# Optimization experiments

Hardware: AMD Instinct MI355X
Metric: run time of the kernel (lower is better)

The kernel has to match this reference:

```python
import jax, jax.numpy as jnp
from jax import lax
import numpy as np

B, N = 64, 128           # graphs per batch, nodes per graph
MAX_LEVEL = 3
N_TRUNKS, TRUNK_LEN = 32, 32
H, OUT = 256, 10


def setup_inputs() -> dict:
    key = jax.random.key(0)
    ks = jax.random.split(key, 12)
    batch_feature = jax.random.normal(ks[0], (B, N), dtype=jnp.float32)
    trunk_idx = jax.random.randint(ks[1], (MAX_LEVEL, N_TRUNKS, TRUNK_LEN), 0, N, dtype=jnp.int32)
    trunk_len = jax.random.randint(ks[2], (MAX_LEVEL, N_TRUNKS), 1, TRUNK_LEN + 1, dtype=jnp.int32)
    s = 1.0 / np.sqrt(H)
    W_enc = jax.random.uniform(ks[3], (1, H), jnp.float32, -1.0, 1.0)
    b_enc = jax.random.uniform(ks[4], (H,), jnp.float32, -1.0, 1.0)
    W_ih = jax.random.uniform(ks[5], (MAX_LEVEL, 4 * H, H), jnp.float32, -s, s)
    W_hh = jax.random.uniform(ks[6], (MAX_LEVEL, 4 * H, H), jnp.float32, -s, s)
    b_ih = jax.random.uniform(ks[7], (MAX_LEVEL, 4 * H), jnp.float32, -s, s)
    b_hh = jax.random.uniform(ks[8], (MAX_LEVEL, 4 * H), jnp.float32, -s, s)
    W_lin = jax.random.uniform(ks[9], (MAX_LEVEL, H, OUT), jnp.float32, -s, s)
    b_lin = jax.random.uniform(ks[10], (MAX_LEVEL, OUT), jnp.float32, -s, s)
    return {"batch_feature": batch_feature, "trunk_idx": trunk_idx, "trunk_len": trunk_len,
            "W_enc": W_enc, "b_enc": b_enc, "W_ih": W_ih, "W_hh": W_hh,
            "b_ih": b_ih, "b_hh": b_hh, "W_lin": W_lin, "b_lin": b_lin}


def _lstm_scan(seq, W_ih, W_hh, b):
    """seq: [L, M, H] -> all hidden states [L, M, H] (single-layer LSTM, PyTorch gate order i,f,g,o)."""
    M = seq.shape[1]
    Hd = W_hh.shape[1]
    def step(carry, x_t):
        h, c = carry
        gates = x_t @ W_ih.T + h @ W_hh.T + b   # [M, 4H]
        i, f, g, o = jnp.split(gates, 4, axis=-1)
        c = jax.nn.sigmoid(f) * c + jax.nn.sigmoid(i) * jnp.tanh(g)
        h = jax.nn.sigmoid(o) * jnp.tanh(c)
        return (h, c), h
    init = (jnp.zeros((M, Hd), seq.dtype), jnp.zeros((M, Hd), seq.dtype))
    _, hs = lax.scan(step, init, seq)
    return hs


def reference(batch_feature, trunk_idx, trunk_len, W_enc, b_enc, W_ih, W_hh, b_ih, b_hh, W_lin, b_lin):
    Bv, Nv = batch_feature.shape
    Hd = W_enc.shape[1]
    # node encoder on scalar features: x [B*N, 1] @ W_enc [1, H]
    x_attr = (batch_feature.reshape(-1, 1) @ W_enc + b_enc).reshape(Bv, Nv, Hd)
    trunk_len = jnp.maximum(trunk_len, 1)
    score = jnp.zeros((Bv, W_lin.shape[-1]), x_attr.dtype)
    for l in range(trunk_idx.shape[0]):
        idx = trunk_idx[l]                       # [T, L]
        T, L = idx.shape
        seqs = x_attr[:, idx]                    # gather trunks -> [B, T, L, H]
        seqs = seqs.reshape(Bv * T, L, Hd).transpose(1, 0, 2)   # [L, B*T, H]
        hs = _lstm_scan(seqs, W_ih[l], W_hh[l], b_ih[l] + b_hh[l])  # [L, B*T, H]
        lens = jnp.tile(trunk_len[l], Bv)        # [B*T]
        h_last = hs[lens - 1, jnp.arange(Bv * T)]   # hidden at last valid step (== packed h_n)
        h_trunk = h_last.reshape(Bv, T, Hd).sum(axis=1)  # scatter-sum per graph (indices are i repeated T times)
        score = score + h_trunk @ W_lin[l] + b_lin[l]
    return score


if __name__ == "__main__":
    out = reference(**setup_inputs())
    print(out.shape, out.dtype)
```

## Files before the change

kernel.cpp:

```cpp
#include <hip/hip_runtime.h>
#include <hip/hip_bf16.h>
#include <stdint.h>

#define B_   64
#define N_   128
#define H_   256
#define FH   1024
#define NT   32
#define TL   32
#define LV   3
#define OUT_ 10
#define NTRK 96
#define UNITS 384
#define NWORK 256

typedef __attribute__((ext_vector_type(4))) int   int4v;
typedef __attribute__((ext_vector_type(4))) float f32x4;

#define QW  (0.0625f / 127.0f)
#define QH  (1.0f / 127.0f)
#define QS  (QW * QH)
#define L2E 1.442695041f
#define QSI (-L2E * QS)
#define QSG (2.0f * L2E * QS)
#define C2  (2.0f * L2E)

__device__ inline float exp2f_(float x) { return __builtin_amdgcn_exp2f(x); }
__device__ inline float rcpf_(float x)  { return __builtin_amdgcn_rcpf(x); }

__global__ void prep_all(const float* __restrict__ W_enc, const float* __restrict__ b_enc,
                         const float* __restrict__ W_ih, const float* __restrict__ b_ih,
                         const float* __restrict__ b_hh, const float* __restrict__ W_hh,
                         const float* __restrict__ b_lin, const int* __restrict__ trunk_len,
                         float* __restrict__ u, float* __restrict__ v,
                         char* __restrict__ whh_i8, float* __restrict__ out,
                         int* __restrict__ sorted, int* __restrict__ counter) {
    int blk = blockIdx.x;
    int tid = threadIdx.x;
    if (blk < 768) {
        int j = blk * 4 + (tid >> 6);
        int lane = tid & 63;
        const float4 w  = ((const float4*)(W_ih + (size_t)j * H_))[lane];
        const float4 we = ((const float4*)W_enc)[lane];
        const float4 be = ((const float4*)b_enc)[lane];
        float du = w.x * we.x + w.y * we.y + w.z * we.z + w.w * we.w;
        float dv = w.x * be.x + w.y * be.y + w.z * be.z + w.w * be.w;
        for (int m = 32; m >= 1; m >>= 1) { du += __shfl_xor(du, m); dv += __shfl_xor(dv, m); }
        if (lane == 0) {
            int g = (j & 1023) >> 8;
            float s = (g == 2) ? (2.0f * L2E) : (-L2E);
            u[j] = s * du;
            v[j] = s * (dv + b_ih[j] + b_hh[j]);
        }
    } else if (blk < 1536) {
        int gid = (blk - 768) * 256 + tid;
        const float4 w = ((const float4*)W_hh)[gid];
        char4 o;
        int a0 = __float2int_rn(w.x * (127.0f / 0.0625f));
        int a1 = __float2int_rn(w.y * (127.0f / 0.0625f));
        int a2 = __float2int_rn(w.z * (127.0f / 0.0625f));
        int a3 = __float2int_rn(w.w * (127.0f / 0.0625f));
        a0 = a0 > 127 ? 127 : (a0 < -127 ? -127 : a0);
        a1 = a1 > 127 ? 127 : (a1 < -127 ? -127 : a1);
        a2 = a2 > 127 ? 127 : (a2 < -127 ? -127 : a2);
        a3 = a3 > 127 ? 127 : (a3 < -127 ? -127 : a3);
        o.x = (char)a0; o.y = (char)a1; o.z = (char)a2; o.w = (char)a3;
        ((char4*)whh_i8)[gid] = o;
        if (gid < B_ * OUT_) {
            int oo = gid % OUT_;
            out[gid] = b_lin[oo] + b_lin[OUT_ + oo] + b_lin[2 * OUT_ + oo];
        }
    } else {
        if (tid < NTRK) {
            int li = trunk_len[tid]; if (li < 1) li = 1;
            int rank = 0;
            for (int j2 = 0; j2 < NTRK; ++j2) {
                int lj = trunk_len[j2]; if (lj < 1) lj = 1;
                rank += (lj > li) || (lj == li && j2 < tid);
            }
            sorted[rank] = tid;
        }
        if (tid == 0) *counter = 0;
    }
}

__global__ __launch_bounds__(1024) __attribute__((amdgpu_waves_per_eu(4, 4)))
void lstm_main(const float* __restrict__ bfeat, const int* __restrict__ trunk_idx,
               const int* __restrict__ trunk_len,
               const char* __restrict__ whh_i8,
               const float* __restrict__ u, const float* __restrict__ v,
               const float* __restrict__ W_lin, const int* __restrict__ sorted,
               int* __restrict__ counter, float* __restrict__ out) {
    __shared__ __align__(16) char hbuf[2][16][272];
    __shared__ __align__(16) float sbuf[2][16];
    __shared__ int sh_uid;

    const int tid = threadIdx.x;
    const int w = tid >> 6;
    const int lane = tid & 63;
    const int col = lane & 15;
    const int q = lane >> 4;

    int4v z4; z4[0] = 0; z4[1] = 0; z4[2] = 0; z4[3] = 0;
    asm volatile("" : "+v"(z4));

    for (;;) {
        if (tid == 0) sh_uid = atomicAdd(counter, 1);
        __syncthreads();
        const int uid = sh_uid;
        if (uid >= UNITS) break;

        const int r = uid >> 2, qq = uid & 3;
        const int tt = sorted[r];
        const int l = tt >> 5;
        const int b0 = qq * 16;

        int len = trunk_len[tt];
        if (len < 1) len = 1;
        const int* tix = trunk_idx + tt * TL;
        const char* whh_l = whh_i8 + (size_t)l * FH * H_;

        int4v Breg[4][4];
        #pragma unroll
        for (int g = 0; g < 4; ++g) {
            int j = g * 256 + w * 16 + col;
            const char* bp = whh_l + (size_t)j * H_ + q * 16;
            #pragma unroll
            for (int k = 0; k < 4; ++k)
                Breg[g][k] = *(const int4v*)(bp + k * 64);
        }

        float u_r[4], v_r[4];
        {
            const float* u_l = u + l * FH;
            const float* v_l = v + l * FH;
            #pragma unroll
            for (int g = 0; g < 4; ++g) {
                int j = g * 256 + w * 16 + col;
                u_r[g] = u_l[j];
                v_r[g] = v_l[j];
            }
        }

        float c_r[4];

        if (tid < 16) sbuf[0][tid] = bfeat[(b0 + tid) * N_ + tix[0]];
        __syncthreads();

        {
            if (len > 1 && tid < 16) sbuf[1][tid] = bfeat[(b0 + tid) * N_ + tix[1]];
            f32x4 sv = *(const f32x4*)&sbuf[0][q * 4];
            #pragma unroll
            for (int rg = 0; rg < 4; ++rg) {
                float xi = fmaf(sv[rg], u_r[0], v_r[0]);
                float xg = fmaf(sv[rg], u_r[2], v_r[2]);
                float xo = fmaf(sv[rg], u_r[3], v_r[3]);
                float si = rcpf_(exp2f_(xi) + 1.0f);
                float so = rcpf_(exp2f_(xo) + 1.0f);
                float tg = fmaf(-2.0f, rcpf_(exp2f_(xg) + 1.0f), 1.0f);
                float cn = si * tg;
                c_r[rg] = cn;
                float th127 = fmaf(-254.0f, rcpf_(exp2f_(C2 * cn) + 1.0f), 127.0f);
                hbuf[1][q * 4 + rg][w * 16 + col] = (char)__float2int_rn(so * th127);
            }
            __syncthreads();
        }

        for (int p = 1; p < len; ++p) {
            #pragma unroll
            for (int g = 0; g < 4; ++g)
                asm volatile("" : "+v"(Breg[g][0]), "+v"(Breg[g][1]),
                                  "+v"(Breg[g][2]), "+v"(Breg[g][3]));

            const int ri = p & 1, wi = ri ^ 1;

            if (p + 1 < len && tid < 16)
                sbuf[wi][tid] = bfeat[(b0 + tid) * N_ + tix[p + 1]];

            int4v a_f[4];
            #pragma unroll
            for (int k = 0; k < 4; ++k)
                a_f[k] = *(const int4v*)&hbuf[ri][col][k * 64 + q * 16];

            f32x4 sv = *(const f32x4*)&sbuf[ri][q * 4];

            int4v acc[4];
            #pragma unroll
            for (int g = 0; g < 4; ++g) {
                acc[g] = __builtin_amdgcn_mfma_i32_16x16x64_i8(a_f[0], Breg[g][0], z4, 0, 0, 0);
                #pragma unroll
                for (int k = 1; k < 4; ++k)
                    acc[g] = __builtin_amdgcn_mfma_i32_16x16x64_i8(a_f[k], Breg[g][k], acc[g], 0, 0, 0);
            }

            #pragma unroll
            for (int rg = 0; rg < 4; ++rg) {
                float xi = fmaf((float)acc[0][rg], QSI, fmaf(sv[rg], u_r[0], v_r[0]));
                float xf = fmaf((float)acc[1][rg], QSI, fmaf(sv[rg], u_r[1], v_r[1]));
                float xg = fmaf((float)acc[2][rg], QSG, fmaf(sv[rg], u_r[2], v_r[2]));
                float xo = fmaf((float)acc[3][rg], QSI, fmaf(sv[rg], u_r[3], v_r[3]));
                float si = rcpf_(exp2f_(xi) + 1.0f);
                float sf = rcpf_(exp2f_(xf) + 1.0f);
                float so = rcpf_(exp2f_(xo) + 1.0f);
                float tg = fmaf(-2.0f, rcpf_(exp2f_(xg) + 1.0f), 1.0f);
                float cn = fmaf(sf, c_r[rg], si * tg);
                c_r[rg] = cn;
                float th127 = fmaf(-254.0f, rcpf_(exp2f_(C2 * cn) + 1.0f), 127.0f);
                hbuf[wi][q * 4 + rg][w * 16 + col] = (char)__float2int_rn(so * th127);
            }

            __syncthreads();
        }

        const char (*hl)[272] = hbuf[len & 1];
        const float* wl = W_lin + l * H_ * OUT_;
        if (tid < 16 * OUT_) {
            int m = tid / OUT_, o = tid % OUT_;
            float s = 0.f;
            for (int k = 0; k < H_; ++k)
                s += (float)hl[m][k] * QH * wl[k * OUT_ + o];
            atomicAdd(&out[(b0 + m) * OUT_ + o], s);
        }
    }
}

extern "C" void kernel_launch(void* const* d_in, const int* in_sizes, int n_in,
                              void* d_out, int out_size, void* d_ws, size_t ws_size,
                              hipStream_t stream) {
    const float* bfeat = (const float*)d_in[0];
    const int*   tidx  = (const int*)d_in[1];
    const int*   tlen  = (const int*)d_in[2];
    const float* W_enc = (const float*)d_in[3];
    const float* b_enc = (const float*)d_in[4];
    const float* W_ih  = (const float*)d_in[5];
    const float* W_hh  = (const float*)d_in[6];
    const float* b_ih  = (const float*)d_in[7];
    const float* b_hh  = (const float*)d_in[8];
    const float* W_lin = (const float*)d_in[9];
    const float* b_lin = (const float*)d_in[10];
    float* out = (float*)d_out;

    char*  whh_i8 = (char*)d_ws;
    float* u = (float*)((char*)d_ws + 786432);
    float* v = (float*)((char*)d_ws + 786432 + 12288);
    int* sorted  = (int*)((char*)d_ws + 811008);
    int* counter = (int*)((char*)d_ws + 811392);

    prep_all<<<1537, 256, 0, stream>>>(W_enc, b_enc, W_ih, b_ih, b_hh, W_hh, b_lin,
                                       tlen, u, v, whh_i8, out, sorted, counter);
    lstm_main<<<NWORK, 1024, 0, stream>>>(bfeat, tidx, tlen, whh_i8, u, v, W_lin,
                                          sorted, counter, out);
}
```

Before: 150.4 us.

## Stage half of int8 W_hh in LDS and stream the other half from global each step

Instead of keeping all 64 KB-per-wave int8 W_hh fragments pinned in registers, the kernel copies gates i and f (512 rows) into a 136 KB LDS buffer per unit and reloads gates g and o from global/L2 memory on every timestep. This frees many VGPRs, but adds LDS reads and repeated global loads inside the serial recurrence. The big shared buffer also limits each CU to one block, and the per-step global loads sit on the latency-critical path.

```diff
diff --git a/kernel.cpp b/kernel.cpp
--- a/kernel.cpp
+++ b/kernel.cpp
@@ -13,6 +13,7 @@
 #define NTRK 96
 #define UNITS 384
 #define NWORK 256
+#define WST  272
 
 typedef __attribute__((ext_vector_type(4))) int   int4v;
 typedef __attribute__((ext_vector_type(4))) float f32x4;
@@ -91,6 +92,7 @@
                const float* __restrict__ u, const float* __restrict__ v,
                const float* __restrict__ W_lin, const int* __restrict__ sorted,
                int* __restrict__ counter, float* __restrict__ out) {
+    __shared__ __align__(16) char wbuf[512][WST];
     __shared__ __align__(16) char hbuf[2][16][272];
     __shared__ __align__(16) float sbuf[2][16];
     __shared__ int sh_uid;
@@ -120,14 +122,12 @@
         const int* tix = trunk_idx + tt * TL;
         const char* whh_l = whh_i8 + (size_t)l * FH * H_;
 
-        int4v Breg[4][4];
-        #pragma unroll
-        for (int g = 0; g < 4; ++g) {
-            int j = g * 256 + w * 16 + col;
-            const char* bp = whh_l + (size_t)j * H_ + q * 16;
-            #pragma unroll
-            for (int k = 0; k < 4; ++k)
-                Breg[g][k] = *(const int4v*)(bp + k * 64);
+        {
+            int row = tid >> 1, half = tid & 1;
+            const int4v* s = (const int4v*)(whh_l + (size_t)row * H_ + half * 128);
+            int4v* d = (int4v*)(&wbuf[row][half * 128]);
+            #pragma unroll
+            for (int i = 0; i < 8; ++i) d[i] = s[i];
         }
 
         float u_r[4], v_r[4];
@@ -167,16 +167,21 @@
         }
 
         for (int p = 1; p < len; ++p) {
-            #pragma unroll
-            for (int g = 0; g < 4; ++g)
-                asm volatile("" : "+v"(Breg[g][0]), "+v"(Breg[g][1]),
-                                  "+v"(Breg[g][2]), "+v"(Breg[g][3]));
-
             const int ri = p & 1, wi = ri ^ 1;
 
             if (p + 1 < len && tid < 16)
                 sbuf[wi][tid] = bfeat[(b0 + tid) * N_ + tix[p + 1]];
 
+            int4v Bs[2][4];
+            #pragma unroll
+            for (int gg = 0; gg < 2; ++gg) {
+                int j = (2 + gg) * 256 + w * 16 + col;
+                const char* bp = whh_l + (size_t)j * H_ + q * 16;
+                #pragma unroll
+                for (int k = 0; k < 4; ++k)
+                    Bs[gg][k] = *(const int4v*)(bp + k * 64);
+            }
+
             int4v a_f[4];
             #pragma unroll
             for (int k = 0; k < 4; ++k)
@@ -186,11 +191,22 @@
 
             int4v acc[4];
             #pragma unroll
-            for (int g = 0; g < 4; ++g) {
-                acc[g] = __builtin_amdgcn_mfma_i32_16x16x64_i8(a_f[0], Breg[g][0], z4, 0, 0, 0);
+            for (int g = 0; g < 2; ++g) {
+                const char* wp = &wbuf[g * 256 + w * 16 + col][q * 16];
+                int4v b0f = *(const int4v*)(wp);
+                acc[g] = __builtin_amdgcn_mfma_i32_16x16x64_i8(a_f[0], b0f, z4, 0, 0, 0);
+                #pragma unroll
+                for (int k = 1; k < 4; ++k) {
+                    int4v bkf = *(const int4v*)(wp + k * 64);
+                    acc[g] = __builtin_amdgcn_mfma_i32_16x16x64_i8(a_f[k], bkf, acc[g], 0, 0, 0);
+                }
+            }
+            #pragma unroll
+            for (int gg = 0; gg < 2; ++gg) {
+                acc[2 + gg] = __builtin_amdgcn_mfma_i32_16x16x64_i8(a_f[0], Bs[gg][0], z4, 0, 0, 0);
                 #pragma unroll
                 for (int k = 1; k < 4; ++k)
-                    acc[g] = __builtin_amdgcn_mfma_i32_16x16x64_i8(a_f[k], Breg[g][k], acc[g], 0, 0, 0);
+                    acc[2 + gg] = __builtin_amdgcn_mfma_i32_16x16x64_i8(a_f[k], Bs[gg][k], acc[2 + gg], 0, 0, 0);
             }
 
             #pragma unroll
```

New measurement: 152.7 us. About the same (+1.5%).
